# Optimization experiments

Measured on AMD Instinct MI355X. Metric: run time of the kernel, lower is better.

The kernel has to match this reference:

```python
import jax, jax.numpy as jnp
import numpy as np


def conv2d(x, w, b=None, pad=0):
    # x: [N,C,H,W], w: [O,I,kh,kw] (cross-correlation, matches torch conv2d)
    out = jax.lax.conv_general_dilated(
        x, w, window_strides=(1, 1), padding=[(pad, pad), (pad, pad)],
        dimension_numbers=('NCHW', 'OIHW', 'NCHW'))
    if b is not None:
        out = out + b[None, :, None, None]
    return out


def se_block(f, w1, b1, w2, b2):
    # squeeze-excite: global avg pool -> 1x1 conv -> relu -> 1x1 conv -> sigmoid
    s = jnp.mean(f, axis=(2, 3), keepdims=True)
    s = jax.nn.relu(conv2d(s, w1, b1, pad=0))
    s = jax.nn.sigmoid(conv2d(s, w2, b2, pad=0))
    return f * s


def setup_inputs() -> dict:
    key = jax.random.key(0)
    ks = jax.random.split(key, 32)
    B, C, H, W = 8, 3, 128, 128
    F_, S, K = 128, 8, 72  # features, squeeze, n basis kernels
    rn = lambda k, shp, sc=0.05: (jax.random.normal(k, shp, dtype=jnp.float32) * sc)
    return {
        'x': jax.random.normal(ks[0], (B, C, H, W), dtype=jnp.float32),
        'w_head': rn(ks[1], (F_, C, 3, 3)), 'b_head': rn(ks[2], (F_,)),
        'w_h1a': rn(ks[3], (F_, F_, 3, 3)), 'b_h1a': rn(ks[4], (F_,)),
        'w_h1b': rn(ks[5], (F_, F_, 3, 3)), 'b_h1b': rn(ks[6], (F_,)),
        'du1_w1': rn(ks[7], (S, F_, 1, 1)), 'du1_b1': rn(ks[8], (S,)),
        'du1_w2': rn(ks[9], (F_, S, 1, 1)), 'du1_b2': rn(ks[10], (F_,)),
        'w_h2a': rn(ks[11], (F_, F_, 3, 3)), 'b_h2a': rn(ks[12], (F_,)),
        'w_h2b': rn(ks[13], (F_, F_, 3, 3)), 'b_h2b': rn(ks[14], (F_,)),
        'du2_w1': rn(ks[15], (S, F_, 1, 1)), 'du2_b1': rn(ks[16], (S,)),
        'du2_w2': rn(ks[17], (F_, S, 1, 1)), 'du2_b2': rn(ks[18], (F_,)),
        'w_tail': rn(ks[19], (K, F_, 3, 3)), 'b_tail': rn(ks[20], (K,)),
        'kernel': rn(ks[21], (K, 1, 5, 5), 0.2),  # fixed 72x5x5 basis
    }


def reference(x, w_head, b_head, w_h1a, b_h1a, w_h1b, b_h1b,
              du1_w1, du1_b1, du1_w2, du1_b2,
              w_h2a, b_h2a, w_h2b, b_h2b,
              du2_w1, du2_b1, du2_w2, du2_b2,
              w_tail, b_tail, kernel):
    B, C, H, W = x.shape
    K = kernel.shape[0]
    # trunk: head -> (conv relu)x2 -> SE -> (conv relu)x2 -> SE -> tail
    f = conv2d(x, w_head, b_head, pad=1)
    f = jax.nn.relu(conv2d(f, w_h1a, b_h1a, pad=1))
    f = jax.nn.relu(conv2d(f, w_h1b, b_h1b, pad=1))
    f = se_block(f, du1_w1, du1_b1, du1_w2, du1_b2)
    f = jax.nn.relu(conv2d(f, w_h2a, b_h2a, pad=1))
    f = jax.nn.relu(conv2d(f, w_h2b, b_h2b, pad=1))
    f = se_block(f, du2_w1, du2_b1, du2_w2, du2_b2)
    wgt = conv2d(f, w_tail, b_tail, pad=1).reshape(B, 1, K, H, W)
    # dynamic filtering: apply 72 fixed 5x5 basis kernels per channel, then
    # per-pixel weighted sum over the 72 basis responses
    xp = jnp.pad(x, ((0, 0), (0, 0), (2, 2), (2, 2)), mode='reflect')
    xp = xp.reshape(B * C, 1, H + 4, W + 4)
    x_com = conv2d(xp, kernel, None, pad=0).reshape(B, C, K, H, W)
    out = jnp.sum(wgt * x_com, axis=2)  # [B,3,H,W]
    return out
```

## Files before the change

### kernel.cpp

```cpp
#include <hip/hip_runtime.h>
#include <math.h>


typedef __attribute__((ext_vector_type(8))) short bf16x8;
typedef __attribute__((ext_vector_type(4))) float f32x4;

__device__ inline float bf2f(unsigned short u) {
    unsigned v = ((unsigned)u) << 16;
    return __builtin_bit_cast(float, v);
}
__device__ inline unsigned short f2bf(float f) {
    unsigned u = __builtin_bit_cast(unsigned, f);
    u += 0x7FFF + ((u >> 16) & 1);
    return (unsigned short)(u >> 16);
}

__global__ __launch_bounds__(256) void head_conv(
    const float* __restrict__ x, const float* __restrict__ w,
    const float* __restrict__ bias, unsigned short* __restrict__ out)
{
    __shared__ float wlds[216];
    __shared__ float tile[3][34 * 34];
    const int tid = threadIdx.x, cog = blockIdx.y, b = blockIdx.z;
    const int tile_y = (blockIdx.x >> 2) * 32, tile_x = (blockIdx.x & 3) * 32;

    if (tid < 216) {
        int co = tid & 7, rest = tid >> 3, tap = rest % 9, ci = rest / 9;
        wlds[tid] = w[((cog * 8 + co) * 3 + ci) * 9 + tap];
    }
    for (int idx = tid; idx < 3 * 34 * 34; idx += 256) {
        int ci = idx / 1156, rem = idx - ci * 1156;
        int r = rem / 34, c = rem - r * 34;
        int gy = tile_y - 1 + r, gx = tile_x - 1 + c;
        float v = 0.f;
        if ((unsigned)gy < 128u && (unsigned)gx < 128u)
            v = x[(((size_t)(b * 3 + ci)) << 14) + (gy << 7) + gx];
        tile[ci][rem] = v;
    }
    __syncthreads();

    const int ty = tid >> 4, tx = tid & 15, py = ty * 2;
    float acc[2][2][8];
    #pragma unroll
    for (int r = 0; r < 2; ++r)
        #pragma unroll
        for (int h = 0; h < 2; ++h)
            #pragma unroll
            for (int co = 0; co < 8; ++co) acc[r][h][co] = 0.f;

    #pragma unroll
    for (int ci = 0; ci < 3; ++ci) {
        #pragma unroll
        for (int ky = 0; ky < 3; ++ky) {
            #pragma unroll
            for (int kx = 0; kx < 3; ++kx) {
                const float* wp = wlds + (ci * 9 + ky * 3 + kx) * 8;
                float i00 = tile[ci][(py + ky) * 34 + tx + kx];
                float i01 = tile[ci][(py + ky) * 34 + tx + 16 + kx];
                float i10 = tile[ci][(py + 1 + ky) * 34 + tx + kx];
                float i11 = tile[ci][(py + 1 + ky) * 34 + tx + 16 + kx];
                #pragma unroll
                for (int co = 0; co < 8; ++co) {
                    float wv = wp[co];
                    acc[0][0][co] += i00 * wv;
                    acc[0][1][co] += i01 * wv;
                    acc[1][0][co] += i10 * wv;
                    acc[1][1][co] += i11 * wv;
                }
            }
        }
    }

    #pragma unroll
    for (int r = 0; r < 2; ++r) {
        #pragma unroll
        for (int h = 0; h < 2; ++h) {
            int gy = tile_y + py + r, gx = tile_x + tx + h * 16;
            bf16x8 pv;
            #pragma unroll
            for (int co = 0; co < 8; ++co)
                pv[co] = (short)f2bf(acc[r][h][co] + bias[cog * 8 + co]);
            *(bf16x8*)(out + (((((size_t)b << 14) + gy * 128 + gx)) << 7) + cog * 8) = pv;
        }
    }
}

template <int LM, int NTW, int WNSPLIT, int DOMEAN, int TAILFUSE>
__global__ __launch_bounds__(256, 2) void conv_mfma(
    const unsigned short* __restrict__ in, const unsigned short* __restrict__ wT,
    size_t wstride, const float* __restrict__ bias, unsigned short* __restrict__ out,
    float* __restrict__ meanb, const float* __restrict__ x,
    const unsigned short* __restrict__ kb, float* __restrict__ outf,
    int Coutp, int Cout, int relu)
{
    __shared__ unsigned short lds[TAILFUSE ? 256 * 104 : 324 * 64];
    const int tid = threadIdx.x;
    const int b = blockIdx.y;
    const int row0 = (blockIdx.x >> 3) << 4;
    const int col0 = (blockIdx.x & 7) << 4;
    const int l = tid & 63, wv = tid >> 6;
    const int li = l & 15, lq = l >> 4;
    const int m_base = WNSPLIT ? (wv >> 1) * LM : wv * LM;
    const int n_base = WNSPLIT ? (wv & 1) * NTW : 0;
    const size_t inb = ((size_t)b) << 14;
    const unsigned short* wbase = wT + (size_t)b * wstride;

    f32x4 acc[LM][NTW];
    #pragma unroll
    for (int lm = 0; lm < LM; ++lm)
        #pragma unroll
        for (int nt = 0; nt < NTW; ++nt)
            acc[lm][nt] = (f32x4){0.f, 0.f, 0.f, 0.f};

    #pragma unroll 1
    for (int half = 0; half < 2; ++half) {
        __syncthreads();
        for (int u = tid; u < 2592; u += 256) {
            int px = u >> 3, g = u & 7;
            int hr = px / 18, hc = px - hr * 18;
            int gy = row0 - 1 + hr, gx = col0 - 1 + hc;
            bf16x8 v = {0, 0, 0, 0, 0, 0, 0, 0};
            if ((unsigned)gy < 128u && (unsigned)gx < 128u)
                v = *(const bf16x8*)(in + ((inb + (gy << 7) + gx) << 7) + half * 64 + g * 8);
            int p = g ^ (px & 7);
            *(bf16x8*)(lds + px * 64 + p * 8) = v;
        }
        __syncthreads();

        auto loadB = [&](bf16x8 (&dst)[NTW], int s) {
            int tap = s >> 1, kcl = s & 1;
            const unsigned short* p = wbase +
                (size_t)(tap * 4 + half * 2 + kcl) * (Coutp * 32) +
                (n_base * 16 + li) * 32 + lq * 8;
            #pragma unroll
            for (int nt = 0; nt < NTW; ++nt)
                dst[nt] = *(const bf16x8*)(p + nt * 512);
        };
        auto compute = [&](bf16x8 (&bf)[NTW], int s) {
            int tap = s >> 1, kcl = s & 1;
            int ky = tap / 3, kx = tap - ky * 3;
            int g = kcl * 4 + lq;
            #pragma unroll
            for (int lm = 0; lm < LM; ++lm) {
                int px = (m_base + lm + ky) * 18 + li + kx;
                bf16x8 af = *(const bf16x8*)(lds + px * 64 + ((g ^ (px & 7)) * 8));
                #pragma unroll
                for (int nt = 0; nt < NTW; ++nt)
                    acc[lm][nt] = __builtin_amdgcn_mfma_f32_16x16x32_bf16(
                        af, bf[nt], acc[lm][nt], 0, 0, 0);
            }
        };

        bf16x8 bufA[NTW], bufB[NTW];
        loadB(bufA, 0);
        #pragma unroll 1
        for (int it = 0; it < 18; it += 2) {
            loadB(bufB, it + 1);
            compute(bufA, it);
            if (it + 2 < 18) loadB(bufA, it + 2);
            compute(bufB, it + 1);
        }
    }

    float bv[NTW], msum[NTW];
    #pragma unroll
    for (int nt = 0; nt < NTW; ++nt) {
        int co = (n_base + nt) * 16 + li;
        bv[nt] = (co < Cout) ? bias[co] : 0.f;
        msum[nt] = 0.f;
    }

    if (TAILFUSE) {
        __syncthreads();
        #pragma unroll
        for (int lm = 0; lm < LM; ++lm) {
            int rowl = m_base + lm;
            #pragma unroll
            for (int r = 0; r < 4; ++r) {
                int coll = lq * 4 + r;
                #pragma unroll
                for (int nt = 0; nt < NTW; ++nt)
                    lds[(rowl * 16 + coll) * 104 + nt * 16 + li] =
                        f2bf(acc[lm][nt][r] + bv[nt]);
            }
        }
        {
            bf16x8 z = {0, 0, 0, 0, 0, 0, 0, 0};
            *(bf16x8*)(lds + tid * 104 + 80) = z;
            *(bf16x8*)(lds + tid * 104 + 88) = z;
        }
        __syncthreads();

        f32x4 eacc[4][2];
        #pragma unroll
        for (int mm = 0; mm < 4; ++mm)
            #pragma unroll
            for (int nt = 0; nt < 2; ++nt)
                eacc[mm][nt] = (f32x4){0.f, 0.f, 0.f, 0.f};
        #pragma unroll
        for (int s = 0; s < 3; ++s) {
            bf16x8 kbf[2];
            #pragma unroll
            for (int nt = 0; nt < 2; ++nt)
                kbf[nt] = *(const bf16x8*)(kb + ((s * 2 + nt) * 16 + li) * 32 + lq * 8);
            #pragma unroll
            for (int mm = 0; mm < 4; ++mm) {
                int px = (wv * 4 + mm) * 16 + li;
                bf16x8 pf = *(const bf16x8*)(lds + px * 104 + s * 32 + lq * 8);
                #pragma unroll
                for (int nt = 0; nt < 2; ++nt)
                    eacc[mm][nt] = __builtin_amdgcn_mfma_f32_16x16x32_bf16(
                        pf, kbf[nt], eacc[mm][nt], 0, 0, 0);
            }
        }
        __syncthreads();

        float* elds = (float*)lds;
        #pragma unroll
        for (int mm = 0; mm < 4; ++mm) {
            #pragma unroll
            for (int nt = 0; nt < 2; ++nt) {
                int i = nt * 16 + li;
                if (i < 25) {
                    #pragma unroll
                    for (int r = 0; r < 4; ++r) {
                        int px = (wv * 4 + mm) * 16 + lq * 4 + r;
                        elds[px * 33 + i] = eacc[mm][nt][r];
                    }
                }
            }
        }
        __syncthreads();

        const int h = row0 + (tid >> 4), w = col0 + (tid & 15);
        const int pix = h * 128 + w;
        float e[25];
        #pragma unroll
        for (int i = 0; i < 25; ++i) e[i] = elds[tid * 33 + i];

        int yy[5], xx[5];
        #pragma unroll
        for (int d = 0; d < 5; ++d) {
            int y = h - 2 + d;
            yy[d] = y < 0 ? -y : (y > 127 ? 254 - y : y);
            int xv = w - 2 + d;
            xx[d] = xv < 0 ? -xv : (xv > 127 ? 254 - xv : xv);
        }
        #pragma unroll
        for (int c = 0; c < 3; ++c) {
            const float* xc = x + ((size_t)(b * 3 + c) << 14);
            float s = 0.f;
            #pragma unroll
            for (int dy = 0; dy < 5; ++dy)
                #pragma unroll
                for (int dx = 0; dx < 5; ++dx)
                    s += e[dy * 5 + dx] * xc[yy[dy] * 128 + xx[dx]];
            outf[((size_t)(b * 3 + c) << 14) + pix] = s;
        }
        return;
    }

    #pragma unroll
    for (int lm = 0; lm < LM; ++lm) {
        int row = row0 + m_base + lm;
        #pragma unroll
        for (int r = 0; r < 4; ++r) {
            int col = col0 + lq * 4 + r;
            size_t pbase = (inb + row * 128 + col) * (size_t)Coutp;
            #pragma unroll
            for (int nt = 0; nt < NTW; ++nt) {
                float v = acc[lm][nt][r] + bv[nt];
                if (relu) v = fmaxf(v, 0.f);
                if (DOMEAN) msum[nt] += v;
                out[pbase + (n_base + nt) * 16 + li] = f2bf(v);
            }
        }
    }
    if (DOMEAN) {
        #pragma unroll
        for (int nt = 0; nt < NTW; ++nt) {
            float t = msum[nt];
            t += __shfl_xor(t, 16, 64);
            t += __shfl_xor(t, 32, 64);
            if (lq == 0)
                atomicAdd(&meanb[b * 128 + (n_base + nt) * 16 + li], t);
        }
    }
}

__device__ inline void wtrans_one(const float* w, unsigned short* wT,
                                  int Co, int Coutp, int idx)
{
    int ch = idx & 31;
    int rest = idx >> 5;
    int co = rest % Coutp;
    int slice = rest / Coutp;
    int kc = slice & 3, tap = slice >> 2;
    float v = (co < Co) ? w[((size_t)(co * 128 + kc * 32 + ch)) * 9 + tap] : 0.f;
    wT[idx] = f2bf(v);
}

__global__ __launch_bounds__(256) void wtrans6(
    const float* __restrict__ w0, const float* __restrict__ w1,
    const float* __restrict__ w2, const float* __restrict__ w3,
    const float* __restrict__ w4, const float* __restrict__ kern,
    unsigned short* __restrict__ t0, unsigned short* __restrict__ t1,
    unsigned short* __restrict__ t2, unsigned short* __restrict__ t3,
    unsigned short* __restrict__ t4, unsigned short* __restrict__ kb)
{
    int idx = blockIdx.x * 256 + threadIdx.x;
    int y = blockIdx.y;
    if (y < 4) {
        const float* w = y == 0 ? w0 : y == 1 ? w1 : y == 2 ? w2 : w3;
        unsigned short* t = y == 0 ? t0 : y == 1 ? t1 : y == 2 ? t2 : t3;
        wtrans_one(w, t, 128, 128, idx);
    } else if (y == 4) {
        if (idx < 9 * 4 * 80 * 32) wtrans_one(w4, t4, 72, 80, idx);
    } else {
        if (idx < 3072) {
            int lq = (idx & 31) >> 3, j = idx & 7;
            int row = idx >> 5;
            int li = row & 15, snt = row >> 4;
            int s = snt >> 1, nt = snt & 1;
            int co = s * 32 + lq * 8 + j, i = nt * 16 + li;
            float v = (co < 72 && i < 25) ? kern[co * 25 + i] : 0.f;
            kb[idx] = f2bf(v);
        }
    }
}

__global__ __launch_bounds__(256) void wscale8f(
    const unsigned short* __restrict__ wT, const float* __restrict__ meanb,
    const float* __restrict__ w1, const float* __restrict__ b1,
    const float* __restrict__ w2, const float* __restrict__ b2,
    unsigned short* __restrict__ out, int Coutp)
{
    const int b = blockIdx.y, c = threadIdx.x;
    __shared__ float h1[8];
    __shared__ float sl[128];
    if (c < 8) {
        float s = 0.f;
        for (int j = 0; j < 128; ++j) s += w1[c * 128 + j] * meanb[b * 128 + j];
        h1[c] = fmaxf(s * (1.f / 16384.f) + b1[c], 0.f);
    }
    __syncthreads();
    if (c < 128) {
        float s = b2[c];
        #pragma unroll
        for (int j = 0; j < 8; ++j) s += w2[c * 8 + j] * h1[j];
        sl[c] = 1.f / (1.f + expf(-s));
    }
    __syncthreads();
    int r = blockIdx.x * 256 + c;
    int ch = r & 31;
    int kc = ((r >> 5) / Coutp) & 3;
    out[(size_t)b * (9 * 4 * Coutp * 32) + r] = f2bf(bf2f(wT[r]) * sl[kc * 32 + ch]);
}

extern "C" void kernel_launch(void* const* d_in, const int* in_sizes, int n_in,
                              void* d_out, int out_size, void* d_ws, size_t ws_size,
                              hipStream_t stream)
{
    const float* x      = (const float*)d_in[0];
    const float* w_head = (const float*)d_in[1];
    const float* b_head = (const float*)d_in[2];
    const float* w_h1a  = (const float*)d_in[3];
    const float* b_h1a  = (const float*)d_in[4];
    const float* w_h1b  = (const float*)d_in[5];
    const float* b_h1b  = (const float*)d_in[6];
    const float* du1_w1 = (const float*)d_in[7];
    const float* du1_b1 = (const float*)d_in[8];
    const float* du1_w2 = (const float*)d_in[9];
    const float* du1_b2 = (const float*)d_in[10];
    const float* w_h2a  = (const float*)d_in[11];
    const float* b_h2a  = (const float*)d_in[12];
    const float* w_h2b  = (const float*)d_in[13];
    const float* b_h2b  = (const float*)d_in[14];
    const float* du2_w1 = (const float*)d_in[15];
    const float* du2_b1 = (const float*)d_in[16];
    const float* du2_w2 = (const float*)d_in[17];
    const float* du2_b2 = (const float*)d_in[18];
    const float* w_tail = (const float*)d_in[19];
    const float* b_tail = (const float*)d_in[20];
    const float* kern   = (const float*)d_in[21];
    float* out = (float*)d_out;

    unsigned short* fb0  = (unsigned short*)d_ws;
    unsigned short* fb1  = fb0 + 16777216;
    unsigned short* wt1  = fb1 + 16777216;
    unsigned short* wt2  = wt1 + 147456;
    unsigned short* wt3  = wt2 + 147456;
    unsigned short* wt4  = wt3 + 147456;
    unsigned short* wtt  = wt4 + 147456;
    unsigned short* wsa  = wtt + 92160;
    unsigned short* wst  = wsa + 8 * 147456;
    unsigned short* kbb  = wst + 8 * 92160;
    float* mean1  = (float*)(kbb + 3072);
    float* mean2  = mean1 + 1024;

    dim3 blk(256);
    hipMemsetAsync(mean1, 0, 8192, stream);

    wtrans6<<<dim3(576, 6), blk, 0, stream>>>(w_h1a, w_h1b, w_h2a, w_h2b, w_tail,
                                              kern, wt1, wt2, wt3, wt4, wtt, kbb);

    head_conv<<<dim3(16, 16, 8), blk, 0, stream>>>(x, w_head, b_head, fb0);

    dim3 cgrid(64, 8);
    conv_mfma<8, 4, 1, 0, 0><<<cgrid, blk, 0, stream>>>(
        fb0, wt1, 0, b_h1a, fb1, nullptr, nullptr, nullptr, nullptr, 128, 128, 1);
    conv_mfma<8, 4, 1, 1, 0><<<cgrid, blk, 0, stream>>>(
        fb1, wt2, 0, b_h1b, fb0, mean1, nullptr, nullptr, nullptr, 128, 128, 1);

    wscale8f<<<dim3(576, 8), blk, 0, stream>>>(wt3, mean1, du1_w1, du1_b1,
                                               du1_w2, du1_b2, wsa, 128);

    conv_mfma<8, 4, 1, 0, 0><<<cgrid, blk, 0, stream>>>(
        fb0, wsa, 147456, b_h2a, fb1, nullptr, nullptr, nullptr, nullptr, 128, 128, 1);
    conv_mfma<8, 4, 1, 1, 0><<<cgrid, blk, 0, stream>>>(
        fb1, wt4, 0, b_h2b, fb0, mean2, nullptr, nullptr, nullptr, 128, 128, 1);

    wscale8f<<<dim3(360, 8), blk, 0, stream>>>(wtt, mean2, du2_w1, du2_b1,
                                               du2_w2, du2_b2, wst, 80);

    conv_mfma<4, 5, 0, 0, 1><<<cgrid, blk, 0, stream>>>(
        fb0, wst, 92160, b_tail, nullptr, nullptr, x, kbb, out, 80, 72, 0);
}
```

Measured before the change: 341.0 us.

## Pad feature maps with zero border and stage input via async global-to-LDS loads

Feature buffers become 130x130 padded images with a zeroed border written by a new small kernel, so the conv staging loop no longer needs bounds checks. The channel blocks inside each pixel are swizzled at store time. Input staging now uses global_load_lds direct copies in four 32-channel quarters with LDS double buffering, and the next quarter is prefetched while the current one computes. This is meant to overlap global loads with MFMA work and cut VGPR round-trips, at the cost of an extra launch, more sync phases and a tighter dependence on the layout.

```diff
diff --git a/kernel.cpp b/kernel.cpp
--- a/kernel.cpp
+++ b/kernel.cpp
@@ -13,6 +13,26 @@
     unsigned u = __builtin_bit_cast(unsigned, f);
     u += 0x7FFF + ((u >> 16) & 1);
     return (unsigned short)(u >> 16);
+}
+
+#define SWKEY(gx) (((gx) >> 1) & 3)
+#define PXB 16900
+
+__global__ __launch_bounds__(256) void zero_border(
+    unsigned short* __restrict__ fb0, unsigned short* __restrict__ fb1)
+{
+    int idx = blockIdx.x * 256 + threadIdx.x;
+    int u = idx & 15;
+    int rest = idx >> 4;
+    int bp = rest % 516;
+    int rb = rest / 516;
+    int b = rb & 7, buf = rb >> 3;
+    int p;
+    if (bp < 130) p = bp;
+    else if (bp < 260) p = 129 * 130 + (bp - 130);
+    else { int k = bp - 260; int r = (k >> 1) + 1; p = r * 130 + ((k & 1) ? 129 : 0); }
+    unsigned short* f = (buf ? fb1 : fb0) + (((size_t)(b * PXB + p)) << 7) + u * 8;
+    *(bf16x8*)f = (bf16x8){0, 0, 0, 0, 0, 0, 0, 0};
 }
 
 __global__ __launch_bounds__(256) void head_conv(
@@ -80,7 +100,8 @@
             #pragma unroll
             for (int co = 0; co < 8; ++co)
                 pv[co] = (short)f2bf(acc[r][h][co] + bias[cog * 8 + co]);
-            *(bf16x8*)(out + (((((size_t)b << 14) + gy * 128 + gx)) << 7) + cog * 8) = pv;
+            int off = (cog >> 2) * 32 + (((cog & 3) ^ SWKEY(gx + 1)) << 3);
+            *(bf16x8*)(out + (((size_t)(b * PXB + (gy + 1) * 130 + gx + 1)) << 7) + off) = pv;
         }
     }
 }
@@ -93,7 +114,7 @@
     const unsigned short* __restrict__ kb, float* __restrict__ outf,
     int Coutp, int Cout, int relu)
 {
-    __shared__ unsigned short lds[TAILFUSE ? 256 * 104 : 324 * 64];
+    __shared__ unsigned short lds[TAILFUSE ? 26624 : 20736];
     const int tid = threadIdx.x;
     const int b = blockIdx.y;
     const int row0 = (blockIdx.x >> 3) << 4;
@@ -102,7 +123,7 @@
     const int li = l & 15, lq = l >> 4;
     const int m_base = WNSPLIT ? (wv >> 1) * LM : wv * LM;
     const int n_base = WNSPLIT ? (wv & 1) * NTW : 0;
-    const size_t inb = ((size_t)b) << 14;
+    const size_t inb = (size_t)b * PXB;
     const unsigned short* wbase = wT + (size_t)b * wstride;
 
     f32x4 acc[LM][NTW];
@@ -112,54 +133,70 @@
         for (int nt = 0; nt < NTW; ++nt)
             acc[lm][nt] = (f32x4){0.f, 0.f, 0.f, 0.f};
 
+    auto stage = [&](int q) {
+        unsigned short* buf = lds + (q & 1) * 10368;
+        #pragma unroll
+        for (int i = 0; i < 6; ++i) {
+            int u = tid + i * 256;
+            if (u < 1296) {
+                int px = u >> 2, j = u & 3;
+                int hr = px / 18, hc = px - hr * 18;
+                const unsigned short* src =
+                    in + ((inb + (row0 + hr) * 130 + col0 + hc) << 7) + q * 32 + j * 8;
+                __builtin_amdgcn_global_load_lds(
+                    (const __attribute__((address_space(1))) void*)src,
+                    (__attribute__((address_space(3))) void*)(buf + u * 8),
+                    16, 0, 0);
+            }
+        }
+    };
+
+    auto loadB = [&](bf16x8 (&dst)[NTW], int q, int tap) {
+        const unsigned short* p = wbase +
+            (size_t)(tap * 4 + q) * (Coutp * 32) + (n_base * 16 + li) * 32 + lq * 8;
+        #pragma unroll
+        for (int nt = 0; nt < NTW; ++nt)
+            dst[nt] = *(const bf16x8*)(p + nt * 512);
+    };
+    auto compute = [&](const unsigned short* buf, bf16x8 (&bf)[NTW], int tap) {
+        int ky = tap / 3, kx = tap - ky * 3;
+        #pragma unroll
+        for (int lm = 0; lm < LM; ++lm) {
+            int px = (m_base + lm + ky) * 18 + li + kx;
+            int slot = lq ^ SWKEY(col0 + li + kx);
+            bf16x8 af = *(const bf16x8*)(buf + px * 32 + slot * 8);
+            #pragma unroll
+            for (int nt = 0; nt < NTW; ++nt)
+                acc[lm][nt] = __builtin_amdgcn_mfma_f32_16x16x32_bf16(
+                    af, bf[nt], acc[lm][nt], 0, 0, 0);
+        }
+    };
+
+    stage(0);
     #pragma unroll 1
-    for (int half = 0; half < 2; ++half) {
+    for (int q = 0; q < 4; ++q) {
         __syncthreads();
-        for (int u = tid; u < 2592; u += 256) {
-            int px = u >> 3, g = u & 7;
-            int hr = px / 18, hc = px - hr * 18;
-            int gy = row0 - 1 + hr, gx = col0 - 1 + hc;
-            bf16x8 v = {0, 0, 0, 0, 0, 0, 0, 0};
-            if ((unsigned)gy < 128u && (unsigned)gx < 128u)
-                v = *(const bf16x8*)(in + ((inb + (gy << 7) + gx) << 7) + half * 64 + g * 8);
-            int p = g ^ (px & 7);
-            *(bf16x8*)(lds + px * 64 + p * 8) = v;
-        }
-        __syncthreads();
-
-        auto loadB = [&](bf16x8 (&dst)[NTW], int s) {
-            int tap = s >> 1, kcl = s & 1;
-            const unsigned short* p = wbase +
-                (size_t)(tap * 4 + half * 2 + kcl) * (Coutp * 32) +
-                (n_base * 16 + li) * 32 + lq * 8;
-            #pragma unroll
-            for (int nt = 0; nt < NTW; ++nt)
-                dst[nt] = *(const bf16x8*)(p + nt * 512);
-        };
-        auto compute = [&](bf16x8 (&bf)[NTW], int s) {
-            int tap = s >> 1, kcl = s & 1;
-            int ky = tap / 3, kx = tap - ky * 3;
-            int g = kcl * 4 + lq;
-            #pragma unroll
-            for (int lm = 0; lm < LM; ++lm) {
-                int px = (m_base + lm + ky) * 18 + li + kx;
-                bf16x8 af = *(const bf16x8*)(lds + px * 64 + ((g ^ (px & 7)) * 8));
-                #pragma unroll
-                for (int nt = 0; nt < NTW; ++nt)
-                    acc[lm][nt] = __builtin_amdgcn_mfma_f32_16x16x32_bf16(
-                        af, bf[nt], acc[lm][nt], 0, 0, 0);
-            }
-        };
-
-        bf16x8 bufA[NTW], bufB[NTW];
-        loadB(bufA, 0);
-        #pragma unroll 1
-        for (int it = 0; it < 18; it += 2) {
-            loadB(bufB, it + 1);
-            compute(bufA, it);
-            if (it + 2 < 18) loadB(bufA, it + 2);
-            compute(bufB, it + 1);
-        }
+        const unsigned short* buf = lds + (q & 1) * 10368;
+        bf16x8 bA[NTW], bB[NTW];
+        loadB(bA, q, 0);
+        loadB(bB, q, 1);
+        compute(buf, bA, 0);
+        loadB(bA, q, 2);
+        compute(buf, bB, 1);
+        loadB(bB, q, 3);
+        compute(buf, bA, 2);
+        loadB(bA, q, 4);
+        compute(buf, bB, 3);
+        loadB(bB, q, 5);
+        compute(buf, bA, 4);
+        loadB(bA, q, 6);
+        compute(buf, bB, 5);
+        loadB(bB, q, 7);
+        compute(buf, bA, 6);
+        loadB(bA, q, 8);
+        if (q < 3) stage(q + 1);
+        compute(buf, bB, 7);
+        compute(buf, bA, 8);
     }
 
     float bv[NTW], msum[NTW];
@@ -266,13 +303,16 @@
         #pragma unroll
         for (int r = 0; r < 4; ++r) {
             int col = col0 + lq * 4 + r;
-            size_t pbase = (inb + row * 128 + col) * (size_t)Coutp;
+            int key = SWKEY(col + 1);
+            size_t pbase = ((size_t)(inb + (row + 1) * 130 + col + 1)) << 7;
             #pragma unroll
             for (int nt = 0; nt < NTW; ++nt) {
                 float v = acc[lm][nt][r] + bv[nt];
                 if (relu) v = fmaxf(v, 0.f);
                 if (DOMEAN) msum[nt] += v;
-                out[pbase + (n_base + nt) * 16 + li] = f2bf(v);
+                int co = (n_base + nt) * 16 + li;
+                int off = (co & 96) + ((((co >> 3) & 3) ^ key) << 3) + (co & 7);
+                out[pbase + off] = f2bf(v);
             }
         }
     }
@@ -385,9 +425,10 @@
     const float* kern   = (const float*)d_in[21];
     float* out = (float*)d_out;
 
+    const size_t FBN = (size_t)8 * PXB * 128;
     unsigned short* fb0  = (unsigned short*)d_ws;
-    unsigned short* fb1  = fb0 + 16777216;
-    unsigned short* wt1  = fb1 + 16777216;
+    unsigned short* fb1  = fb0 + FBN;
+    unsigned short* wt1  = fb1 + FBN;
     unsigned short* wt2  = wt1 + 147456;
     unsigned short* wt3  = wt2 + 147456;
     unsigned short* wt4  = wt3 + 147456;
@@ -400,6 +441,7 @@
 
     dim3 blk(256);
     hipMemsetAsync(mean1, 0, 8192, stream);
+    zero_border<<<516, blk, 0, stream>>>(fb0, fb1);
 
     wtrans6<<<dim3(576, 6), blk, 0, stream>>>(w_h1a, w_h1b, w_h2a, w_h2b, w_tail,
                                               kern, wt1, wt2, wt3, wt4, wtt, kbb);
```

After: 414.8 us. +21.6%, slower.
